# Kernel tuning notes

Hardware: AMD Instinct MI355X
Metric: run time of the kernel (lower is better)

## Reference

```python
import jax, jax.numpy as jnp
import numpy as np

B, NK, U = 4096, 128, 256


def setup_inputs() -> dict:
    key = jax.random.key(0)
    ks = jax.random.split(key, 10)
    s = 1.0 / np.sqrt(U)
    sf = 1.0 / np.sqrt(2 * U)
    return {
        "query": jax.random.normal(ks[0], (B, U), jnp.float32),
        "keys": jax.random.normal(ks[1], (B, NK, U), jnp.float32),
        "Wq": jax.random.uniform(ks[2], (U, U), jnp.float32, -s, s),
        "bq": jnp.zeros((U,), jnp.float32),
        "Wk": jax.random.uniform(ks[3], (U, U), jnp.float32, -s, s),
        "bk": jnp.zeros((U,), jnp.float32),
        "Wv": jax.random.uniform(ks[4], (U, U), jnp.float32, -s, s),
        "bv": jnp.zeros((U,), jnp.float32),
        "Wf": jax.random.uniform(ks[5], (U, 2 * U), jnp.float32, -sf, sf),
        "bf": jnp.zeros((U,), jnp.float32),
    }


def reference(query, keys, Wq, bq, Wk, bk, Wv, bv, Wf, bf):
    # query: (B,U), keys: (B,NK,U). Batched replacement of the per-key loop.
    q = query @ Wq.T + bq                      # (B,U)
    k = keys @ Wk.T + bk                       # (B,NK,U)
    scores = jnp.einsum('bu,bnu->bn', q, k) / jnp.sqrt(jnp.float32(U))
    p = jax.nn.softmax(scores, axis=-1)        # (B,NK)
    v = keys @ Wv.T + bv                       # (B,NK,U)
    ctx = jnp.einsum('bn,bnu->bu', p, v)       # (B,U)
    fused = jnp.concatenate([ctx, query], axis=-1) @ Wf.T + bf
    return jax.nn.relu(fused)
```

## Files before the change

kernel.cpp:

```cpp
#include <hip/hip_runtime.h>
#include <math.h>

#define U_DIM 256
#define NK_DIM 128
#define B_DIM 4096

__global__ void precompute_kernel(const float* __restrict__ Wq,
                                  const float* __restrict__ bq,
                                  const float* __restrict__ Wk,
                                  const float* __restrict__ Wv,
                                  const float* __restrict__ bv,
                                  const float* __restrict__ Wf,
                                  const float* __restrict__ bf,
                                  float* __restrict__ M1s,
                                  float* __restrict__ c1s,
                                  float* __restrict__ Bd,
                                  float* __restrict__ c2) {
    __shared__ float wqcol[256];
    __shared__ float wfrow[256];
    __shared__ float red[256];
    int l = blockIdx.x, t = threadIdx.x;
    wqcol[t] = Wq[t * 256 + l];
    wfrow[t] = Wf[l * 512 + t];
    __syncthreads();
    float m1 = 0.f, m2 = 0.f;
    for (int i = 0; i < 256; ++i) {
        float wk = Wk[i * 256 + t];
        float wv = Wv[i * 256 + t];
        m1 += wqcol[i] * wk;
        m2 += wfrow[i] * wv;
    }
    M1s[l * 256 + t] = m1 * 0.0625f;
    Bd[t * 256 + l] = m2;
    Bd[(256 + t) * 256 + l] = Wf[l * 512 + 256 + t];
    red[t] = wfrow[t] * bv[t];
    __syncthreads();
    for (int s = 128; s > 0; s >>= 1) {
        if (t < s) red[t] += red[t + s];
        __syncthreads();
    }
    if (t == 0) c2[l] = red[0] + bf[l];
    if (l == 0) {
        float c1 = 0.f;
        for (int i = 0; i < 256; ++i) c1 += bq[i] * Wk[i * 256 + t];
        c1s[t] = c1 * 0.0625f;
    }
}

__global__ void qk_kernel(const float* __restrict__ query,
                          const float* __restrict__ M1s,
                          const float* __restrict__ c1s,
                          float* __restrict__ qk) {
    __shared__ __align__(16) float qs[8][256];
    int t = threadIdx.x;
    int b0 = blockIdx.x * 8;
    #pragma unroll
    for (int r = 0; r < 8; ++r) qs[r][t] = query[(size_t)(b0 + r) * 256 + t];
    __syncthreads();
    float acc[8] = {0.f, 0.f, 0.f, 0.f, 0.f, 0.f, 0.f, 0.f};
    #pragma unroll 2
    for (int k0 = 0; k0 < 256; k0 += 4) {
        float b0v = M1s[(k0 + 0) * 256 + t];
        float b1v = M1s[(k0 + 1) * 256 + t];
        float b2v = M1s[(k0 + 2) * 256 + t];
        float b3v = M1s[(k0 + 3) * 256 + t];
        #pragma unroll
        for (int r = 0; r < 8; ++r) {
            float4 a = *(const float4*)&qs[r][k0];
            acc[r] += a.x * b0v + a.y * b1v + a.z * b2v + a.w * b3v;
        }
    }
    float c1 = c1s[t];
    #pragma unroll
    for (int r = 0; r < 8; ++r) qk[(size_t)(b0 + r) * 256 + t] = acc[r] + c1;
}

__global__ __launch_bounds__(256) void attn_kernel(const float* __restrict__ keys,
                                                   const float* __restrict__ qk,
                                                   float* __restrict__ kctx) {
    int b = blockIdx.x;
    int t = threadIdx.x;
    int lane = t & 63;
    int w = t >> 6;
    const float4* K4 = (const float4*)keys + (size_t)b * (NK_DIM * U_DIM / 4);
    float4 q4 = ((const float4*)qk)[(size_t)b * 64 + lane];
    __shared__ float s_sc[32];
    __shared__ float s_L[4];
    __shared__ __align__(16) float4 s_acc[4][64];
    float m = -INFINITY, L = 0.f;
    float4 acc = {0.f, 0.f, 0.f, 0.f};
    for (int c = 0; c < 4; ++c) {
        int n0 = c * 32 + w * 8;
        float4 kv[8];
        #pragma unroll
        for (int r = 0; r < 8; ++r) kv[r] = K4[(n0 + r) * 64 + lane];
        #pragma unroll
        for (int r = 0; r < 8; ++r) {
            float s = kv[r].x * q4.x + kv[r].y * q4.y + kv[r].z * q4.z + kv[r].w * q4.w;
            #pragma unroll
            for (int msk = 32; msk > 0; msk >>= 1) s += __shfl_xor(s, msk, 64);
            if (lane == r) s_sc[w * 8 + r] = s;
        }
        __syncthreads();
        float cmax = -INFINITY;
        #pragma unroll
        for (int i = 0; i < 32; ++i) cmax = fmaxf(cmax, s_sc[i]);
        float nm = fmaxf(m, cmax);
        float scale = __expf(m - nm);
        m = nm;
        L *= scale;
        acc.x *= scale; acc.y *= scale; acc.z *= scale; acc.w *= scale;
        #pragma unroll
        for (int r = 0; r < 8; ++r) {
            float p = __expf(s_sc[w * 8 + r] - nm);
            L += p;
            acc.x += p * kv[r].x; acc.y += p * kv[r].y;
            acc.z += p * kv[r].z; acc.w += p * kv[r].w;
        }
        __syncthreads();
    }
    s_acc[w][lane] = acc;
    if (lane == 0) s_L[w] = L;
    __syncthreads();
    if (w == 0) {
        float4 a0 = s_acc[0][lane], a1 = s_acc[1][lane];
        float4 a2 = s_acc[2][lane], a3 = s_acc[3][lane];
        float inv = 1.f / (s_L[0] + s_L[1] + s_L[2] + s_L[3]);
        float4 o;
        o.x = (a0.x + a1.x + a2.x + a3.x) * inv;
        o.y = (a0.y + a1.y + a2.y + a3.y) * inv;
        o.z = (a0.z + a1.z + a2.z + a3.z) * inv;
        o.w = (a0.w + a1.w + a2.w + a3.w) * inv;
        ((float4*)kctx)[(size_t)b * 64 + lane] = o;
    }
}

__global__ void out_kernel(const float* __restrict__ kctx,
                           const float* __restrict__ query,
                           const float* __restrict__ Bd,
                           const float* __restrict__ c2,
                           float* __restrict__ out) {
    __shared__ __align__(16) float as[8][512];
    int t = threadIdx.x;
    int b0 = blockIdx.x * 8;
    #pragma unroll
    for (int r = 0; r < 8; ++r) {
        as[r][t] = kctx[(size_t)(b0 + r) * 256 + t];
        as[r][256 + t] = query[(size_t)(b0 + r) * 256 + t];
    }
    __syncthreads();
    float acc[8] = {0.f, 0.f, 0.f, 0.f, 0.f, 0.f, 0.f, 0.f};
    #pragma unroll 2
    for (int k0 = 0; k0 < 512; k0 += 4) {
        float b0v = Bd[(k0 + 0) * 256 + t];
        float b1v = Bd[(k0 + 1) * 256 + t];
        float b2v = Bd[(k0 + 2) * 256 + t];
        float b3v = Bd[(k0 + 3) * 256 + t];
        #pragma unroll
        for (int r = 0; r < 8; ++r) {
            float4 a = *(const float4*)&as[r][k0];
            acc[r] += a.x * b0v + a.y * b1v + a.z * b2v + a.w * b3v;
        }
    }
    float c = c2[t];
    #pragma unroll
    for (int r = 0; r < 8; ++r)
        out[(size_t)(b0 + r) * 256 + t] = fmaxf(acc[r] + c, 0.f);
}

extern "C" void kernel_launch(void* const* d_in, const int* in_sizes, int n_in,
                              void* d_out, int out_size, void* d_ws, size_t ws_size,
                              hipStream_t stream) {
    const float* query = (const float*)d_in[0];
    const float* keys  = (const float*)d_in[1];
    const float* Wq    = (const float*)d_in[2];
    const float* bq    = (const float*)d_in[3];
    const float* Wk    = (const float*)d_in[4];
    const float* Wv    = (const float*)d_in[6];
    const float* bv    = (const float*)d_in[7];
    const float* Wf    = (const float*)d_in[8];
    const float* bf    = (const float*)d_in[9];
    float* out = (float*)d_out;

    float* ws   = (float*)d_ws;
    float* M1s  = ws;
    float* c1s  = M1s + 65536;
    float* Bd   = c1s + 256;
    float* c2   = Bd + 131072;
    float* qk   = c2 + 256;
    float* kctx = qk + 4096 * 256;

    hipLaunchKernelGGL(precompute_kernel, dim3(256), dim3(256), 0, stream,
                       Wq, bq, Wk, Wv, bv, Wf, bf, M1s, c1s, Bd, c2);
    hipLaunchKernelGGL(qk_kernel, dim3(512), dim3(256), 0, stream,
                       query, M1s, c1s, qk);
    hipLaunchKernelGGL(attn_kernel, dim3(4096), dim3(256), 0, stream,
                       keys, qk, kctx);
    hipLaunchKernelGGL(out_kernel, dim3(512), dim3(256), 0, stream,
                       kctx, query, Bd, c2, out);
}
```

Measured before the change: 881.8 us.

## Give each wave its own key slice with per-wave softmax and double-buffered loads

The attention kernel now assigns each wave a contiguous block of 32 keys and keeps its own running max and sum. This removes the per-chunk shared-memory score exchange and the two block barriers per chunk. The partial results are merged once at the end with max-rescaled weights. Key loads are double-buffered in two register arrays using nontemporal loads, so the next 8 rows are fetched while the current 8 are processed. The cost is higher register pressure, which may lower occupancy in this memory-bound kernel.

```diff
diff --git a/kernel.cpp b/kernel.cpp
--- a/kernel.cpp
+++ b/kernel.cpp
@@ -4,6 +4,8 @@
 #define U_DIM 256
 #define NK_DIM 128
 #define B_DIM 4096
+
+typedef float nvf4 __attribute__((ext_vector_type(4)));
 
 __global__ void precompute_kernel(const float* __restrict__ Wq,
                                   const float* __restrict__ bq,
@@ -82,55 +84,69 @@
     int t = threadIdx.x;
     int lane = t & 63;
     int w = t >> 6;
-    const float4* K4 = (const float4*)keys + (size_t)b * (NK_DIM * U_DIM / 4);
+    const nvf4* K4 = (const nvf4*)keys + (size_t)b * (NK_DIM * U_DIM / 4)
+                     + (size_t)(w * 32) * 64 + lane;
     float4 q4 = ((const float4*)qk)[(size_t)b * 64 + lane];
-    __shared__ float s_sc[32];
-    __shared__ float s_L[4];
-    __shared__ __align__(16) float4 s_acc[4][64];
     float m = -INFINITY, L = 0.f;
     float4 acc = {0.f, 0.f, 0.f, 0.f};
-    for (int c = 0; c < 4; ++c) {
-        int n0 = c * 32 + w * 8;
-        float4 kv[8];
-        #pragma unroll
-        for (int r = 0; r < 8; ++r) kv[r] = K4[(n0 + r) * 64 + lane];
-        #pragma unroll
-        for (int r = 0; r < 8; ++r) {
-            float s = kv[r].x * q4.x + kv[r].y * q4.y + kv[r].z * q4.z + kv[r].w * q4.w;
+
+    nvf4 ka[8], kb[8];
+
+    auto load8 = [&](nvf4* kv, int base) {
+        #pragma unroll
+        for (int r = 0; r < 8; ++r)
+            kv[r] = __builtin_nontemporal_load(K4 + (base + r) * 64);
+    };
+    auto proc8 = [&](const nvf4* kv) {
+        float s[8];
+        #pragma unroll
+        for (int r = 0; r < 8; ++r) {
+            float d = kv[r].x * q4.x + kv[r].y * q4.y + kv[r].z * q4.z + kv[r].w * q4.w;
             #pragma unroll
-            for (int msk = 32; msk > 0; msk >>= 1) s += __shfl_xor(s, msk, 64);
-            if (lane == r) s_sc[w * 8 + r] = s;
-        }
-        __syncthreads();
-        float cmax = -INFINITY;
-        #pragma unroll
-        for (int i = 0; i < 32; ++i) cmax = fmaxf(cmax, s_sc[i]);
+            for (int msk = 32; msk > 0; msk >>= 1) d += __shfl_xor(d, msk, 64);
+            s[r] = d;
+        }
+        float cmax = fmaxf(fmaxf(fmaxf(s[0], s[1]), fmaxf(s[2], s[3])),
+                           fmaxf(fmaxf(s[4], s[5]), fmaxf(s[6], s[7])));
         float nm = fmaxf(m, cmax);
-        float scale = __expf(m - nm);
+        float sc = __expf(m - nm);
         m = nm;
-        L *= scale;
-        acc.x *= scale; acc.y *= scale; acc.z *= scale; acc.w *= scale;
-        #pragma unroll
-        for (int r = 0; r < 8; ++r) {
-            float p = __expf(s_sc[w * 8 + r] - nm);
+        L *= sc;
+        acc.x *= sc; acc.y *= sc; acc.z *= sc; acc.w *= sc;
+        #pragma unroll
+        for (int r = 0; r < 8; ++r) {
+            float p = __expf(s[r] - nm);
             L += p;
             acc.x += p * kv[r].x; acc.y += p * kv[r].y;
             acc.z += p * kv[r].z; acc.w += p * kv[r].w;
         }
-        __syncthreads();
-    }
+    };
+
+    load8(ka, 0);
+    load8(kb, 8);  proc8(ka);
+    load8(ka, 16); proc8(kb);
+    load8(kb, 24); proc8(ka);
+    proc8(kb);
+
+    __shared__ __align__(16) float4 s_acc[4][64];
+    __shared__ float s_m[4];
+    __shared__ float s_L[4];
     s_acc[w][lane] = acc;
-    if (lane == 0) s_L[w] = L;
+    if (lane == 0) { s_m[w] = m; s_L[w] = L; }
     __syncthreads();
     if (w == 0) {
+        float m0 = s_m[0], m1 = s_m[1], m2 = s_m[2], m3 = s_m[3];
+        float ms = fmaxf(fmaxf(m0, m1), fmaxf(m2, m3));
+        float w0 = __expf(m0 - ms), w1 = __expf(m1 - ms);
+        float w2 = __expf(m2 - ms), w3 = __expf(m3 - ms);
+        float inv = 1.f / (s_L[0] * w0 + s_L[1] * w1 + s_L[2] * w2 + s_L[3] * w3);
         float4 a0 = s_acc[0][lane], a1 = s_acc[1][lane];
         float4 a2 = s_acc[2][lane], a3 = s_acc[3][lane];
-        float inv = 1.f / (s_L[0] + s_L[1] + s_L[2] + s_L[3]);
         float4 o;
-        o.x = (a0.x + a1.x + a2.x + a3.x) * inv;
-        o.y = (a0.y + a1.y + a2.y + a3.y) * inv;
-        o.z = (a0.z + a1.z + a2.z + a3.z) * inv;
-        o.w = (a0.w + a1.w + a2.w + a3.w) * inv;
+        o.x = (a0.x * w0 + a1.x * w1 + a2.x * w2 + a3.x * w3) * inv;
+        o.y = (a0.y * w0 + a1.y * w1 + a2.y * w2 + a3.y * w3) * inv;
+        o.z = (a0.z * w0 + a1.z * w1 + a2.z * w2 + a3.z * w3) * inv;
+        o.w = (a0.w * w0 + a1.w * w1 + a2.w * w2 + a3.w * w3) * inv;
         ((float4*)kctx)[(size_t)b * 64 + lane] = o;
     }
 }
```

Result: faster. 816.1 us (-7.5%).
